# Optimization experiments

Hardware: AMD Instinct MI355X
Metric: run time of the kernel (lower is better)

## Reference

```python
import jax, jax.numpy as jnp
import numpy as np

VOCAB, HIDDEN = 128, 1024
BATCH, SEQ = 64, 512


def setup_inputs() -> dict:
    key = jax.random.key(0)
    ks = jax.random.split(key, 6)
    scale = 1.0 / np.sqrt(HIDDEN)
    return {
        "x": jax.random.randint(ks[0], (BATCH, SEQ), 0, VOCAB, dtype=jnp.int32),
        "h": jnp.zeros((BATCH, HIDDEN), dtype=jnp.float32),
        "emb": jax.random.normal(ks[1], (VOCAB, HIDDEN), dtype=jnp.float32),
        "W_hx": jax.random.normal(ks[2], (HIDDEN, HIDDEN), dtype=jnp.float32) * scale,
        "b_hx": jnp.zeros((HIDDEN,), dtype=jnp.float32),
        "W_hh": jax.random.normal(ks[3], (HIDDEN, HIDDEN), dtype=jnp.float32) * scale,
        "W_out": jax.random.normal(ks[4], (HIDDEN, VOCAB), dtype=jnp.float32) * scale,
        "b_out": jnp.zeros((VOCAB,), dtype=jnp.float32),
    }


def reference(x, h, emb, W_hx, b_hx, W_hh, W_out, b_out):
    # x: [B, S] int indices; h: [B, H] initial hidden state
    x_emb = emb[x]  # [B, S, H] embedding lookup

    def step(h, xt):  # xt: [B, H]
        h_new = jnp.tanh(xt @ W_hx + b_hx + h @ W_hh)
        return h_new, h_new

    # scan over time axis (sequential dependency on h)
    h_final, hs = jax.lax.scan(step, h, jnp.swapaxes(x_emb, 0, 1))  # hs: [S, B, H]
    out = jnp.swapaxes(hs, 0, 1)  # [B, S, H]
    logits = out @ W_out + b_out  # [B, S, V]
    return logits, h_final
```

## Files before the change

### kernel.cpp

```cpp
#include <hip/hip_runtime.h>
#include <stdint.h>
#include <stddef.h>

#define VOCAB  128
#define HIDDEN 1024
#define BATCH  64
#define SEQ    512

#define NGROUP 4
#define BG     16
#define NWG    32
#define CJ     32
#define NVW    4
#define NTHR   512

#define POISON 0x7F800000u

#define E2_OFF   0
#define WOT_OFF  131072
#define BUF_OFF  196608

typedef __attribute__((ext_vector_type(8))) short short8_t;
typedef __attribute__((ext_vector_type(4))) float f32x4;

__device__ __forceinline__ uint4 cload4u(const void* p) {
    uint4 v;
    asm volatile("global_load_dwordx4 %0, %1, off sc0 sc1" : "=v"(v) : "v"(p));
    return v;
}
__device__ __forceinline__ void cstoreu(unsigned int* p, unsigned int x) {
    asm volatile("global_store_dword %0, %1, off sc0 sc1" :: "v"(p), "v"(x) : "memory");
}
#define WAITVM0() asm volatile("s_waitcnt vmcnt(0)" ::: "memory")
#define SCHED_FENCE() __builtin_amdgcn_sched_barrier(0)

__device__ __forceinline__ unsigned short bf16_rne(float f) {
    unsigned int u = __float_as_uint(f);
    u += 0x7FFF + ((u >> 16) & 1);
    return (unsigned short)(u >> 16);
}
__device__ __forceinline__ float bf16_f32(unsigned short h) {
    return __uint_as_float(((unsigned int)h) << 16);
}

__global__ void e2_kernel(const float* __restrict__ emb, const float* __restrict__ W_hx,
                          const float* __restrict__ b_hx, float* __restrict__ E2) {
    int v = blockIdx.x >> 2;
    int j = (blockIdx.x & 3) * 256 + threadIdx.x;
    const float* er = emb + (size_t)v * HIDDEN;
    float acc = 0.f;
#pragma unroll 8
    for (int k = 0; k < HIDDEN; ++k)
        acc += er[k] * W_hx[(size_t)k * HIDDEN + j];
    E2[(size_t)v * HIDDEN + j] = acc + b_hx[j];
}

__global__ void wot_kernel(const float* __restrict__ W_out, unsigned short* __restrict__ WoT) {
    int v  = blockIdx.x;
    int k4 = threadIdx.x;
    ushort4 r;
    r.x = bf16_rne(W_out[(size_t)(k4*4+0)*VOCAB + v]);
    r.y = bf16_rne(W_out[(size_t)(k4*4+1)*VOCAB + v]);
    r.z = bf16_rne(W_out[(size_t)(k4*4+2)*VOCAB + v]);
    r.w = bf16_rne(W_out[(size_t)(k4*4+3)*VOCAB + v]);
    ((ushort4*)(WoT + (size_t)v * HIDDEN))[k4] = r;
}

__global__ void poison_kernel(unsigned int* __restrict__ bufs) {
    int i = blockIdx.x * 256 + threadIdx.x;
    ((uint4*)bufs)[i] = make_uint4(POISON, POISON, POISON, POISON);
}

extern "C" __global__ void __launch_bounds__(NTHR, 2)
rnn_kernel(const int* __restrict__ x, const float* __restrict__ h0,
           const float* __restrict__ W_hh,
           const float* __restrict__ E2, const unsigned short* __restrict__ WoT,
           const float* __restrict__ b_out,
           unsigned int* __restrict__ bufs,
           float* __restrict__ logits, float* __restrict__ hf) {
    extern __shared__ char lds_raw[];
    short* sHi  = (short*)lds_raw;
    short* sLo  = sHi + 16 * 1024;
    float* sPart = (float*)(sLo + 16 * 1024);
    int*   sX   = (int*)(sPart + 8 * 512);

    const int wg = blockIdx.x;
    const int g  = wg / NWG;
    const int w  = wg % NWG;
    const int b0 = g * BG;
    const int j0 = w * CJ;
    const int tid  = threadIdx.x;
    const int lane = tid & 63;
    const int wv   = tid >> 6;

    {
        const int4* xs4 = (const int4*)(x + (size_t)b0 * SEQ);
#pragma unroll
        for (int i = 0; i < 4; ++i)
            ((int4*)sX)[tid + 512 * i] = xs4[tid + 512 * i];
    }

    short8_t whi[2][4], wlo[2][4];
    {
        const int colb = lane & 15, kgrp = lane >> 4;
#pragma unroll
        for (int ct = 0; ct < 2; ++ct) {
            int col = j0 + ct * 16 + colb;
#pragma unroll
            for (int c = 0; c < 4; ++c) {
                int kb = wv * 128 + c * 32 + kgrp * 8;
#pragma unroll
                for (int e = 0; e < 8; ++e) {
                    float wval = W_hh[(size_t)(kb + e) * HIDDEN + col];
                    unsigned short hi = bf16_rne(wval);
                    whi[ct][c][e] = (short)hi;
                    wlo[ct][c][e] = (short)bf16_rne(wval - bf16_f32(hi));
                }
            }
        }
    }

    short8_t wvo[4];
    {
        const int colv = lane & 15, kgrp = lane >> 4;
#pragma unroll
        for (int c = 0; c < 4; ++c) {
            int kb = wv * 128 + c * 32 + kgrp * 8;
#pragma unroll
            for (int e = 0; e < 8; ++e)
                wvo[c][e] = (colv < NVW)
                    ? (short)WoT[(size_t)(w * NVW + colv) * HIDDEN + kb + e] : (short)0;
        }
    }
    const float boV = (tid < 64) ? b_out[w * NVW + (tid & 3)] : 0.f;
    __syncthreads();

    const int srow = tid >> 5;
    const int sslt = tid & 31;
    const int rb = tid >> 5, jb = tid & 31;
    const int ar = lane & 15, acg = lane >> 4;

    for (int t = 0; t < SEQ; ++t) {
        float e2p = E2[(size_t)sX[rb * SEQ + t] * HIDDEN + j0 + jb];
        if (t == 0) {
#pragma unroll
            for (int i = 0; i < 4; ++i) {
                int c = i * 32 + sslt;
                const float* p = h0 + (size_t)(b0 + srow) * HIDDEN + c * 8;
                short8_t h8, l8;
#pragma unroll
                for (int e = 0; e < 8; ++e) {
                    float vv = p[e];
                    unsigned short hi = bf16_rne(vv);
                    h8[e] = (short)hi;
                    l8[e] = (short)bf16_rne(vv - bf16_f32(hi));
                }
                int cs = (c ^ (srow & 7)) << 3;
                *(short8_t*)(sHi + srow * 1024 + cs) = h8;
                *(short8_t*)(sLo + srow * 1024 + cs) = l8;
            }
        } else {
            const unsigned int* src = bufs + ((size_t)((t - 1) & 3) << 16)
                                           + ((size_t)(b0 + srow) << 10);
            uint4 d[8];
            unsigned pend = 0xF;
            int guard = 0;
            do {
#pragma unroll
                for (int i = 0; i < 4; ++i)
                    if (pend & (1u << i)) {
                        int c = i * 32 + sslt;
                        d[2*i]   = cload4u(src + c * 8);
                        d[2*i+1] = cload4u(src + c * 8 + 4);
                    }
                WAITVM0();
                SCHED_FENCE();
#pragma unroll
                for (int i = 0; i < 4; ++i)
                    if (pend & (1u << i)) {
                        bool ok = d[2*i].x   != POISON && d[2*i].y   != POISON
                               && d[2*i].z   != POISON && d[2*i].w   != POISON
                               && d[2*i+1].x != POISON && d[2*i+1].y != POISON
                               && d[2*i+1].z != POISON && d[2*i+1].w != POISON;
                        if (ok) pend &= ~(1u << i);
                    }
                if (!pend) break;
                __builtin_amdgcn_s_sleep(1);
            } while (++guard < (1 << 20));
            SCHED_FENCE();
#pragma unroll
            for (int i = 0; i < 4; ++i) {
                int c = i * 32 + sslt;
                int cs = (c ^ (srow & 7)) << 3;
                short8_t h8, l8;
                h8[0]=(short)(d[2*i].x>>16);   l8[0]=(short)(d[2*i].x&0xFFFF);
                h8[1]=(short)(d[2*i].y>>16);   l8[1]=(short)(d[2*i].y&0xFFFF);
                h8[2]=(short)(d[2*i].z>>16);   l8[2]=(short)(d[2*i].z&0xFFFF);
                h8[3]=(short)(d[2*i].w>>16);   l8[3]=(short)(d[2*i].w&0xFFFF);
                h8[4]=(short)(d[2*i+1].x>>16); l8[4]=(short)(d[2*i+1].x&0xFFFF);
                h8[5]=(short)(d[2*i+1].y>>16); l8[5]=(short)(d[2*i+1].y&0xFFFF);
                h8[6]=(short)(d[2*i+1].z>>16); l8[6]=(short)(d[2*i+1].z&0xFFFF);
                h8[7]=(short)(d[2*i+1].w>>16); l8[7]=(short)(d[2*i+1].w&0xFFFF);
                *(short8_t*)(sHi + srow * 1024 + cs) = h8;
                *(short8_t*)(sLo + srow * 1024 + cs) = l8;
            }
        }
        __syncthreads();

        f32x4 acc0 = {0.f, 0.f, 0.f, 0.f};
        f32x4 acc1 = {0.f, 0.f, 0.f, 0.f};
#pragma unroll
        for (int c = 0; c < 4; ++c) {
            int c8 = wv * 16 + c * 4 + acg;
            int off = ar * 1024 + ((c8 ^ (ar & 7)) << 3);
            short8_t ahi = *(const short8_t*)(sHi + off);
            short8_t alo = *(const short8_t*)(sLo + off);
            acc0 = __builtin_amdgcn_mfma_f32_16x16x32_bf16(ahi, whi[0][c], acc0, 0, 0, 0);
            acc1 = __builtin_amdgcn_mfma_f32_16x16x32_bf16(ahi, whi[1][c], acc1, 0, 0, 0);
            acc0 = __builtin_amdgcn_mfma_f32_16x16x32_bf16(alo, whi[0][c], acc0, 0, 0, 0);
            acc1 = __builtin_amdgcn_mfma_f32_16x16x32_bf16(alo, whi[1][c], acc1, 0, 0, 0);
            acc0 = __builtin_amdgcn_mfma_f32_16x16x32_bf16(ahi, wlo[0][c], acc0, 0, 0, 0);
            acc1 = __builtin_amdgcn_mfma_f32_16x16x32_bf16(ahi, wlo[1][c], acc1, 0, 0, 0);
        }
#pragma unroll
        for (int q = 0; q < 4; ++q) {
            sPart[wv * 512 + (acg * 4 + q) * 32 + ar]      = acc0[q];
            sPart[wv * 512 + (acg * 4 + q) * 32 + 16 + ar] = acc1[q];
        }
        __syncthreads();

        {
            float s = 0.f;
#pragma unroll
            for (int z = 0; z < 8; ++z) s += sPart[z * 512 + tid];
            float hn = tanhf(s + e2p);
            unsigned short hi = bf16_rne(hn);
            unsigned short lo = bf16_rne(hn - bf16_f32(hi));
            unsigned int pk = ((unsigned int)hi << 16) | (unsigned int)lo;
            size_t idx = ((size_t)(b0 + rb) << 10) + j0 + jb;
            cstoreu(bufs + ((size_t)(t & 3) << 16) + idx, pk);
            cstoreu(bufs + ((size_t)((t + 2) & 3) << 16) + idx, POISON);
            if (t == SEQ - 1)
                hf[(size_t)(b0 + rb) * HIDDEN + j0 + jb] = hn;
        }
        __syncthreads();

        if (t > 0) {
            f32x4 accL = {0.f, 0.f, 0.f, 0.f};
#pragma unroll
            for (int c = 0; c < 4; ++c) {
                int c8 = wv * 16 + c * 4 + acg;
                int off = ar * 1024 + ((c8 ^ (ar & 7)) << 3);
                short8_t ahi = *(const short8_t*)(sHi + off);
                accL = __builtin_amdgcn_mfma_f32_16x16x32_bf16(ahi, wvo[c], accL, 0, 0, 0);
            }
            if (ar < NVW) {
#pragma unroll
                for (int q = 0; q < 4; ++q)
                    sPart[wv * 64 + (acg * 4 + q) * 4 + ar] = accL[q];
            }
            __syncthreads();
            if (tid < 64) {
                int b = tid >> 2, v = tid & 3;
                float s = 0.f;
#pragma unroll
                for (int z = 0; z < 8; ++z) s += sPart[z * 64 + b * 4 + v];
                logits[((size_t)(b0 + b) * SEQ + (t - 1)) * VOCAB + w * NVW + v] = s + boV;
            }
        }
    }

    {
        const unsigned int* src = bufs + ((size_t)((SEQ - 1) & 3) << 16)
                                       + ((size_t)(b0 + srow) << 10);
        uint4 d[8];
        unsigned pend = 0xF;
        int guard = 0;
        do {
#pragma unroll
            for (int i = 0; i < 4; ++i)
                if (pend & (1u << i)) {
                    int c = i * 32 + sslt;
                    d[2*i]   = cload4u(src + c * 8);
                    d[2*i+1] = cload4u(src + c * 8 + 4);
                }
            WAITVM0();
            SCHED_FENCE();
#pragma unroll
            for (int i = 0; i < 4; ++i)
                if (pend & (1u << i)) {
                    bool ok = d[2*i].x   != POISON && d[2*i].y   != POISON
                           && d[2*i].z   != POISON && d[2*i].w   != POISON
                           && d[2*i+1].x != POISON && d[2*i+1].y != POISON
                           && d[2*i+1].z != POISON && d[2*i+1].w != POISON;
                    if (ok) pend &= ~(1u << i);
                }
            if (!pend) break;
            __builtin_amdgcn_s_sleep(1);
        } while (++guard < (1 << 20));
        SCHED_FENCE();
        __syncthreads();
#pragma unroll
        for (int i = 0; i < 4; ++i) {
            int c = i * 32 + sslt;
            int cs = (c ^ (srow & 7)) << 3;
            short8_t h8;
            h8[0]=(short)(d[2*i].x>>16);   h8[1]=(short)(d[2*i].y>>16);
            h8[2]=(short)(d[2*i].z>>16);   h8[3]=(short)(d[2*i].w>>16);
            h8[4]=(short)(d[2*i+1].x>>16); h8[5]=(short)(d[2*i+1].y>>16);
            h8[6]=(short)(d[2*i+1].z>>16); h8[7]=(short)(d[2*i+1].w>>16);
            *(short8_t*)(sHi + srow * 1024 + cs) = h8;
        }
    }
    __syncthreads();
    {
        f32x4 accL = {0.f, 0.f, 0.f, 0.f};
#pragma unroll
        for (int c = 0; c < 4; ++c) {
            int c8 = wv * 16 + c * 4 + acg;
            int off = ar * 1024 + ((c8 ^ (ar & 7)) << 3);
            short8_t ahi = *(const short8_t*)(sHi + off);
            accL = __builtin_amdgcn_mfma_f32_16x16x32_bf16(ahi, wvo[c], accL, 0, 0, 0);
        }
        if (ar < NVW) {
#pragma unroll
            for (int q = 0; q < 4; ++q)
                sPart[wv * 64 + (acg * 4 + q) * 4 + ar] = accL[q];
        }
        __syncthreads();
        if (tid < 64) {
            int b = tid >> 2, v = tid & 3;
            float s = 0.f;
#pragma unroll
            for (int z = 0; z < 8; ++z) s += sPart[z * 64 + b * 4 + v];
            logits[((size_t)(b0 + b) * SEQ + (SEQ - 1)) * VOCAB + w * NVW + v] = s + boV;
        }
    }
}

extern "C" void kernel_launch(void* const* d_in, const int* in_sizes, int n_in,
                              void* d_out, int out_size, void* d_ws, size_t ws_size,
                              hipStream_t stream) {
    (void)in_sizes; (void)n_in; (void)out_size; (void)ws_size;
    const int*   x     = (const int*)  d_in[0];
    const float* h0    = (const float*)d_in[1];
    const float* emb   = (const float*)d_in[2];
    const float* W_hx  = (const float*)d_in[3];
    const float* b_hx  = (const float*)d_in[4];
    const float* W_hh  = (const float*)d_in[5];
    const float* W_out = (const float*)d_in[6];
    const float* b_out = (const float*)d_in[7];

    float* logits = (float*)d_out;
    float* hf     = logits + (size_t)BATCH * SEQ * VOCAB;

    float* ws  = (float*)d_ws;
    float* E2  = ws + E2_OFF;
    unsigned short* WoT = (unsigned short*)(ws + WOT_OFF);
    unsigned int*   bufs = (unsigned int*)(ws + BUF_OFF);

    poison_kernel<<<256, 256, 0, stream>>>(bufs);
    e2_kernel<<<512, 256, 0, stream>>>(emb, W_hx, b_hx, E2);
    wot_kernel<<<128, 256, 0, stream>>>(W_out, WoT);

    hipFuncSetAttribute(reinterpret_cast<const void*>(rnn_kernel),
                        hipFuncAttributeMaxDynamicSharedMemorySize, 114688);
    rnn_kernel<<<NGROUP * NWG, NTHR, 114688, stream>>>(x, h0, W_hh, E2, WoT, b_out,
                                                       bufs, logits, hf);
}
```

Measured before the change: 1.653 ms.

## Double-buffer hidden state in LDS and rotate logits projection across waves

Adds a second LDS buffer for the bf16 hidden-state high parts, alternating by timestep, so the previous step's state stays readable while the next one is written. This lets the per-step output projection run without its own barriers. Instead of every wave computing a partial logits sum and reducing through LDS with two extra __syncthreads, one wave (rotating by timestep) computes the full K=1024 projection from W_out held in LDS and writes logits directly. LDS use rises to about 152 KB, and one wave carries extra MFMA work each step, which may unbalance the waves.

```diff
diff --git a/kernel.cpp b/kernel.cpp
--- a/kernel.cpp
+++ b/kernel.cpp
@@ -79,10 +79,12 @@
            unsigned int* __restrict__ bufs,
            float* __restrict__ logits, float* __restrict__ hf) {
     extern __shared__ char lds_raw[];
-    short* sHi  = (short*)lds_raw;
-    short* sLo  = sHi + 16 * 1024;
-    float* sPart = (float*)(sLo + 16 * 1024);
-    int*   sX   = (int*)(sPart + 8 * 512);
+    short* sHi0 = (short*)lds_raw;
+    short* sHi1 = (short*)(lds_raw + 32768);
+    short* sLo  = (short*)(lds_raw + 65536);
+    float* sPart = (float*)(lds_raw + 98304);
+    short* sWo  = (short*)(lds_raw + 114688);
+    int*   sX   = (int*)(lds_raw + 122880);
 
     const int wg = blockIdx.x;
     const int g  = wg / NWG;
@@ -99,6 +101,11 @@
         for (int i = 0; i < 4; ++i)
             ((int4*)sX)[tid + 512 * i] = xs4[tid + 512 * i];
     }
+    {
+        int r = tid >> 7, cidx = tid & 127;
+        *(short8_t*)(sWo + r * 1024 + cidx * 8) =
+            *(const short8_t*)(WoT + (size_t)(w * NVW + r) * HIDDEN + cidx * 8);
+    }
 
     short8_t whi[2][4], wlo[2][4];
     {
@@ -120,28 +127,17 @@
         }
     }
 
-    short8_t wvo[4];
-    {
-        const int colv = lane & 15, kgrp = lane >> 4;
-#pragma unroll
-        for (int c = 0; c < 4; ++c) {
-            int kb = wv * 128 + c * 32 + kgrp * 8;
-#pragma unroll
-            for (int e = 0; e < 8; ++e)
-                wvo[c][e] = (colv < NVW)
-                    ? (short)WoT[(size_t)(w * NVW + colv) * HIDDEN + kb + e] : (short)0;
-        }
-    }
-    const float boV = (tid < 64) ? b_out[w * NVW + (tid & 3)] : 0.f;
-    __syncthreads();
-
     const int srow = tid >> 5;
     const int sslt = tid & 31;
     const int rb = tid >> 5, jb = tid & 31;
     const int ar = lane & 15, acg = lane >> 4;
+    const float boL = (ar < NVW) ? b_out[w * NVW + ar] : 0.f;
+    __syncthreads();
 
     for (int t = 0; t < SEQ; ++t) {
+        short* sHi_p = (t & 1) ? sHi1 : sHi0;
         float e2p = E2[(size_t)sX[rb * SEQ + t] * HIDDEN + j0 + jb];
+
         if (t == 0) {
 #pragma unroll
             for (int i = 0; i < 4; ++i) {
@@ -156,7 +152,7 @@
                     l8[e] = (short)bf16_rne(vv - bf16_f32(hi));
                 }
                 int cs = (c ^ (srow & 7)) << 3;
-                *(short8_t*)(sHi + srow * 1024 + cs) = h8;
+                *(short8_t*)(sHi_p + srow * 1024 + cs) = h8;
                 *(short8_t*)(sLo + srow * 1024 + cs) = l8;
             }
         } else {
@@ -201,7 +197,7 @@
                 h8[5]=(short)(d[2*i+1].y>>16); l8[5]=(short)(d[2*i+1].y&0xFFFF);
                 h8[6]=(short)(d[2*i+1].z>>16); l8[6]=(short)(d[2*i+1].z&0xFFFF);
                 h8[7]=(short)(d[2*i+1].w>>16); l8[7]=(short)(d[2*i+1].w&0xFFFF);
-                *(short8_t*)(sHi + srow * 1024 + cs) = h8;
+                *(short8_t*)(sHi_p + srow * 1024 + cs) = h8;
                 *(short8_t*)(sLo + srow * 1024 + cs) = l8;
             }
         }
@@ -213,7 +209,7 @@
         for (int c = 0; c < 4; ++c) {
             int c8 = wv * 16 + c * 4 + acg;
             int off = ar * 1024 + ((c8 ^ (ar & 7)) << 3);
-            short8_t ahi = *(const short8_t*)(sHi + off);
+            short8_t ahi = *(const short8_t*)(sHi_p + off);
             short8_t alo = *(const short8_t*)(sLo + off);
             acc0 = __builtin_amdgcn_mfma_f32_16x16x32_bf16(ahi, whi[0][c], acc0, 0, 0, 0);
             acc1 = __builtin_amdgcn_mfma_f32_16x16x32_bf16(ahi, whi[1][c], acc1, 0, 0, 0);
@@ -243,29 +239,32 @@
             if (t == SEQ - 1)
                 hf[(size_t)(b0 + rb) * HIDDEN + j0 + jb] = hn;
         }
-        __syncthreads();
-
-        if (t > 0) {
-            f32x4 accL = {0.f, 0.f, 0.f, 0.f};
-#pragma unroll
-            for (int c = 0; c < 4; ++c) {
-                int c8 = wv * 16 + c * 4 + acg;
-                int off = ar * 1024 + ((c8 ^ (ar & 7)) << 3);
-                short8_t ahi = *(const short8_t*)(sHi + off);
-                accL = __builtin_amdgcn_mfma_f32_16x16x32_bf16(ahi, wvo[c], accL, 0, 0, 0);
+
+        if (t > 0 && wv == ((t - 1) & 7)) {
+            f32x4 L0 = {0.f,0.f,0.f,0.f}, L1 = {0.f,0.f,0.f,0.f};
+            f32x4 L2 = {0.f,0.f,0.f,0.f}, L3 = {0.f,0.f,0.f,0.f};
+            const short8_t zz = {0,0,0,0,0,0,0,0};
+#pragma unroll
+            for (int kq = 0; kq < 8; ++kq) {
+#pragma unroll
+                for (int u = 0; u < 4; ++u) {
+                    int kc = kq * 4 + u;
+                    int c8 = kc * 4 + acg;
+                    short8_t a8 = *(const short8_t*)(sHi_p + ar * 1024 + ((c8 ^ (ar & 7)) << 3));
+                    short8_t b8 = (ar < NVW)
+                        ? *(const short8_t*)(sWo + ar * 1024 + kc * 32 + acg * 8) : zz;
+                    if (u == 0)      L0 = __builtin_amdgcn_mfma_f32_16x16x32_bf16(a8, b8, L0, 0, 0, 0);
+                    else if (u == 1) L1 = __builtin_amdgcn_mfma_f32_16x16x32_bf16(a8, b8, L1, 0, 0, 0);
+                    else if (u == 2) L2 = __builtin_amdgcn_mfma_f32_16x16x32_bf16(a8, b8, L2, 0, 0, 0);
+                    else             L3 = __builtin_amdgcn_mfma_f32_16x16x32_bf16(a8, b8, L3, 0, 0, 0);
+                }
             }
             if (ar < NVW) {
 #pragma unroll
-                for (int q = 0; q < 4; ++q)
-                    sPart[wv * 64 + (acg * 4 + q) * 4 + ar] = accL[q];
-            }
-            __syncthreads();
-            if (tid < 64) {
-                int b = tid >> 2, v = tid & 3;
-                float s = 0.f;
-#pragma unroll
-                for (int z = 0; z < 8; ++z) s += sPart[z * 64 + b * 4 + v];
-                logits[((size_t)(b0 + b) * SEQ + (t - 1)) * VOCAB + w * NVW + v] = s + boV;
+                for (int q = 0; q < 4; ++q) {
+                    float val = L0[q] + L1[q] + L2[q] + L3[q] + boL;
+                    logits[((size_t)(b0 + acg * 4 + q) * SEQ + (t - 1)) * VOCAB + w * NVW + ar] = val;
+                }
             }
         }
     }
@@ -299,7 +298,6 @@
             __builtin_amdgcn_s_sleep(1);
         } while (++guard < (1 << 20));
         SCHED_FENCE();
-        __syncthreads();
 #pragma unroll
         for (int i = 0; i < 4; ++i) {
             int c = i * 32 + sslt;
@@ -309,31 +307,35 @@
             h8[2]=(short)(d[2*i].z>>16);   h8[3]=(short)(d[2*i].w>>16);
             h8[4]=(short)(d[2*i+1].x>>16); h8[5]=(short)(d[2*i+1].y>>16);
             h8[6]=(short)(d[2*i+1].z>>16); h8[7]=(short)(d[2*i+1].w>>16);
-            *(short8_t*)(sHi + srow * 1024 + cs) = h8;
+            *(short8_t*)(sHi0 + srow * 1024 + cs) = h8;
         }
     }
     __syncthreads();
-    {
-        f32x4 accL = {0.f, 0.f, 0.f, 0.f};
-#pragma unroll
-        for (int c = 0; c < 4; ++c) {
-            int c8 = wv * 16 + c * 4 + acg;
-            int off = ar * 1024 + ((c8 ^ (ar & 7)) << 3);
-            short8_t ahi = *(const short8_t*)(sHi + off);
-            accL = __builtin_amdgcn_mfma_f32_16x16x32_bf16(ahi, wvo[c], accL, 0, 0, 0);
+    if (wv == ((SEQ - 1) & 7)) {
+        f32x4 L0 = {0.f,0.f,0.f,0.f}, L1 = {0.f,0.f,0.f,0.f};
+        f32x4 L2 = {0.f,0.f,0.f,0.f}, L3 = {0.f,0.f,0.f,0.f};
+        const short8_t zz = {0,0,0,0,0,0,0,0};
+#pragma unroll
+        for (int kq = 0; kq < 8; ++kq) {
+#pragma unroll
+            for (int u = 0; u < 4; ++u) {
+                int kc = kq * 4 + u;
+                int c8 = kc * 4 + acg;
+                short8_t a8 = *(const short8_t*)(sHi0 + ar * 1024 + ((c8 ^ (ar & 7)) << 3));
+                short8_t b8 = (ar < NVW)
+                    ? *(const short8_t*)(sWo + ar * 1024 + kc * 32 + acg * 8) : zz;
+                if (u == 0)      L0 = __builtin_amdgcn_mfma_f32_16x16x32_bf16(a8, b8, L0, 0, 0, 0);
+                else if (u == 1) L1 = __builtin_amdgcn_mfma_f32_16x16x32_bf16(a8, b8, L1, 0, 0, 0);
+                else if (u == 2) L2 = __builtin_amdgcn_mfma_f32_16x16x32_bf16(a8, b8, L2, 0, 0, 0);
+                else             L3 = __builtin_amdgcn_mfma_f32_16x16x32_bf16(a8, b8, L3, 0, 0, 0);
+            }
         }
         if (ar < NVW) {
 #pragma unroll
-            for (int q = 0; q < 4; ++q)
-                sPart[wv * 64 + (acg * 4 + q) * 4 + ar] = accL[q];
-        }
-        __syncthreads();
-        if (tid < 64) {
-            int b = tid >> 2, v = tid & 3;
-            float s = 0.f;
-#pragma unroll
-            for (int z = 0; z < 8; ++z) s += sPart[z * 64 + b * 4 + v];
-            logits[((size_t)(b0 + b) * SEQ + (SEQ - 1)) * VOCAB + w * NVW + v] = s + boV;
+            for (int q = 0; q < 4; ++q) {
+                float val = L0[q] + L1[q] + L2[q] + L3[q] + boL;
+                logits[((size_t)(b0 + acg * 4 + q) * SEQ + (SEQ - 1)) * VOCAB + w * NVW + ar] = val;
+            }
         }
     }
 }
@@ -364,7 +366,7 @@
     wot_kernel<<<128, 256, 0, stream>>>(W_out, WoT);
 
     hipFuncSetAttribute(reinterpret_cast<const void*>(rnn_kernel),
-                        hipFuncAttributeMaxDynamicSharedMemorySize, 114688);
-    rnn_kernel<<<NGROUP * NWG, NTHR, 114688, stream>>>(x, h0, W_hh, E2, WoT, b_out,
+                        hipFuncAttributeMaxDynamicSharedMemorySize, 155648);
+    rnn_kernel<<<NGROUP * NWG, NTHR, 155648, stream>>>(x, h0, W_hh, E2, WoT, b_out,
                                                        bufs, logits, hf);
 }
```

Result: slower. 1.814 ms (median of 2 runs) (+9.7%).

## Load hidden state directly in MFMA operand layout, bypassing LDS staging

Applied to the files above, without the earlier changes.

Each lane now polls and loads exactly the hidden-state fragments it feeds into the MFMA, so the A operands (hi and lo bf16 parts) stay in registers instead of being written to LDS, synchronized, and read back. The lo-part LDS buffer and the barrier before the recurrent matmul are removed, and the dynamic LDS allocation shrinks. The hi part is still written to LDS for the output-logits projection. Global loads for polling now use a different per-lane access pattern, which may change coalescing.

```diff
diff --git a/kernel.cpp b/kernel.cpp
--- a/kernel.cpp
+++ b/kernel.cpp
@@ -41,6 +41,21 @@
 }
 __device__ __forceinline__ float bf16_f32(unsigned short h) {
     return __uint_as_float(((unsigned int)h) << 16);
+}
+__device__ __forceinline__ bool ok8(const uint4 a, const uint4 b) {
+    return a.x != POISON && a.y != POISON && a.z != POISON && a.w != POISON
+        && b.x != POISON && b.y != POISON && b.z != POISON && b.w != POISON;
+}
+__device__ __forceinline__ void unpack8(const uint4 a, const uint4 b,
+                                        short8_t* h8, short8_t* l8) {
+    (*h8)[0]=(short)(a.x>>16); (*l8)[0]=(short)(a.x&0xFFFF);
+    (*h8)[1]=(short)(a.y>>16); (*l8)[1]=(short)(a.y&0xFFFF);
+    (*h8)[2]=(short)(a.z>>16); (*l8)[2]=(short)(a.z&0xFFFF);
+    (*h8)[3]=(short)(a.w>>16); (*l8)[3]=(short)(a.w&0xFFFF);
+    (*h8)[4]=(short)(b.x>>16); (*l8)[4]=(short)(b.x&0xFFFF);
+    (*h8)[5]=(short)(b.y>>16); (*l8)[5]=(short)(b.y&0xFFFF);
+    (*h8)[6]=(short)(b.z>>16); (*l8)[6]=(short)(b.z&0xFFFF);
+    (*h8)[7]=(short)(b.w>>16); (*l8)[7]=(short)(b.w&0xFFFF);
 }
 
 __global__ void e2_kernel(const float* __restrict__ emb, const float* __restrict__ W_hx,
@@ -80,9 +95,8 @@
            float* __restrict__ logits, float* __restrict__ hf) {
     extern __shared__ char lds_raw[];
     short* sHi  = (short*)lds_raw;
-    short* sLo  = sHi + 16 * 1024;
-    float* sPart = (float*)(sLo + 16 * 1024);
-    int*   sX   = (int*)(sPart + 8 * 512);
+    float* sPart = (float*)(lds_raw + 32768);
+    int*   sX   = (int*)(lds_raw + 49152);
 
     const int wg = blockIdx.x;
     const int g  = wg / NWG;
@@ -92,6 +106,8 @@
     const int tid  = threadIdx.x;
     const int lane = tid & 63;
     const int wv   = tid >> 6;
+    const int r    = lane & 15;
+    const int kg   = lane >> 4;
 
     {
         const int4* xs4 = (const int4*)(x + (size_t)b0 * SEQ);
@@ -102,13 +118,12 @@
 
     short8_t whi[2][4], wlo[2][4];
     {
-        const int colb = lane & 15, kgrp = lane >> 4;
 #pragma unroll
         for (int ct = 0; ct < 2; ++ct) {
-            int col = j0 + ct * 16 + colb;
+            int col = j0 + ct * 16 + r;
 #pragma unroll
             for (int c = 0; c < 4; ++c) {
-                int kb = wv * 128 + c * 32 + kgrp * 8;
+                int kb = wv * 128 + c * 32 + kg * 8;
 #pragma unroll
                 for (int e = 0; e < 8; ++e) {
                     float wval = W_hh[(size_t)(kb + e) * HIDDEN + col];
@@ -122,110 +137,85 @@
 
     short8_t wvo[4];
     {
-        const int colv = lane & 15, kgrp = lane >> 4;
 #pragma unroll
         for (int c = 0; c < 4; ++c) {
-            int kb = wv * 128 + c * 32 + kgrp * 8;
+            int kb = wv * 128 + c * 32 + kg * 8;
 #pragma unroll
             for (int e = 0; e < 8; ++e)
-                wvo[c][e] = (colv < NVW)
-                    ? (short)WoT[(size_t)(w * NVW + colv) * HIDDEN + kb + e] : (short)0;
+                wvo[c][e] = (r < NVW)
+                    ? (short)WoT[(size_t)(w * NVW + r) * HIDDEN + kb + e] : (short)0;
         }
     }
     const float boV = (tid < 64) ? b_out[w * NVW + (tid & 3)] : 0.f;
+    const int rb = tid >> 5, jb = tid & 31;
     __syncthreads();
-
-    const int srow = tid >> 5;
-    const int sslt = tid & 31;
-    const int rb = tid >> 5, jb = tid & 31;
-    const int ar = lane & 15, acg = lane >> 4;
 
     for (int t = 0; t < SEQ; ++t) {
         float e2p = E2[(size_t)sX[rb * SEQ + t] * HIDDEN + j0 + jb];
+
+        short8_t ahi[4], alo[4];
         if (t == 0) {
-#pragma unroll
-            for (int i = 0; i < 4; ++i) {
-                int c = i * 32 + sslt;
-                const float* p = h0 + (size_t)(b0 + srow) * HIDDEN + c * 8;
-                short8_t h8, l8;
+            const float* hr = h0 + ((size_t)(b0 + r) << 10) + wv * 128 + kg * 8;
+#pragma unroll
+            for (int c = 0; c < 4; ++c) {
+                float4 f0 = *(const float4*)(hr + c * 32);
+                float4 f1 = *(const float4*)(hr + c * 32 + 4);
+                float fv[8] = {f0.x,f0.y,f0.z,f0.w,f1.x,f1.y,f1.z,f1.w};
 #pragma unroll
                 for (int e = 0; e < 8; ++e) {
-                    float vv = p[e];
-                    unsigned short hi = bf16_rne(vv);
-                    h8[e] = (short)hi;
-                    l8[e] = (short)bf16_rne(vv - bf16_f32(hi));
+                    unsigned short hi = bf16_rne(fv[e]);
+                    ahi[c][e] = (short)hi;
+                    alo[c][e] = (short)bf16_rne(fv[e] - bf16_f32(hi));
                 }
-                int cs = (c ^ (srow & 7)) << 3;
-                *(short8_t*)(sHi + srow * 1024 + cs) = h8;
-                *(short8_t*)(sLo + srow * 1024 + cs) = l8;
             }
         } else {
             const unsigned int* src = bufs + ((size_t)((t - 1) & 3) << 16)
-                                           + ((size_t)(b0 + srow) << 10);
-            uint4 d[8];
+                                           + ((size_t)(b0 + r) << 10) + wv * 128 + kg * 8;
+            uint4 d0a,d0b,d1a,d1b,d2a,d2b,d3a,d3b;
             unsigned pend = 0xF;
             int guard = 0;
             do {
-#pragma unroll
-                for (int i = 0; i < 4; ++i)
-                    if (pend & (1u << i)) {
-                        int c = i * 32 + sslt;
-                        d[2*i]   = cload4u(src + c * 8);
-                        d[2*i+1] = cload4u(src + c * 8 + 4);
-                    }
+                if (pend & 1u) { d0a = cload4u(src +  0); d0b = cload4u(src +  4); }
+                if (pend & 2u) { d1a = cload4u(src + 32); d1b = cload4u(src + 36); }
+                if (pend & 4u) { d2a = cload4u(src + 64); d2b = cload4u(src + 68); }
+                if (pend & 8u) { d3a = cload4u(src + 96); d3b = cload4u(src + 100); }
                 WAITVM0();
                 SCHED_FENCE();
-#pragma unroll
-                for (int i = 0; i < 4; ++i)
-                    if (pend & (1u << i)) {
-                        bool ok = d[2*i].x   != POISON && d[2*i].y   != POISON
-                               && d[2*i].z   != POISON && d[2*i].w   != POISON
-                               && d[2*i+1].x != POISON && d[2*i+1].y != POISON
-                               && d[2*i+1].z != POISON && d[2*i+1].w != POISON;
-                        if (ok) pend &= ~(1u << i);
-                    }
+                if ((pend & 1u) && ok8(d0a, d0b)) pend &= ~1u;
+                if ((pend & 2u) && ok8(d1a, d1b)) pend &= ~2u;
+                if ((pend & 4u) && ok8(d2a, d2b)) pend &= ~4u;
+                if ((pend & 8u) && ok8(d3a, d3b)) pend &= ~8u;
                 if (!pend) break;
                 __builtin_amdgcn_s_sleep(1);
             } while (++guard < (1 << 20));
             SCHED_FENCE();
-#pragma unroll
-            for (int i = 0; i < 4; ++i) {
-                int c = i * 32 + sslt;
-                int cs = (c ^ (srow & 7)) << 3;
-                short8_t h8, l8;
-                h8[0]=(short)(d[2*i].x>>16);   l8[0]=(short)(d[2*i].x&0xFFFF);
-                h8[1]=(short)(d[2*i].y>>16);   l8[1]=(short)(d[2*i].y&0xFFFF);
-                h8[2]=(short)(d[2*i].z>>16);   l8[2]=(short)(d[2*i].z&0xFFFF);
-                h8[3]=(short)(d[2*i].w>>16);   l8[3]=(short)(d[2*i].w&0xFFFF);
-                h8[4]=(short)(d[2*i+1].x>>16); l8[4]=(short)(d[2*i+1].x&0xFFFF);
-                h8[5]=(short)(d[2*i+1].y>>16); l8[5]=(short)(d[2*i+1].y&0xFFFF);
-                h8[6]=(short)(d[2*i+1].z>>16); l8[6]=(short)(d[2*i+1].z&0xFFFF);
-                h8[7]=(short)(d[2*i+1].w>>16); l8[7]=(short)(d[2*i+1].w&0xFFFF);
-                *(short8_t*)(sHi + srow * 1024 + cs) = h8;
-                *(short8_t*)(sLo + srow * 1024 + cs) = l8;
-            }
-        }
-        __syncthreads();
+            unpack8(d0a, d0b, &ahi[0], &alo[0]);
+            unpack8(d1a, d1b, &ahi[1], &alo[1]);
+            unpack8(d2a, d2b, &ahi[2], &alo[2]);
+            unpack8(d3a, d3b, &ahi[3], &alo[3]);
+        }
+
+#pragma unroll
+        for (int c = 0; c < 4; ++c) {
+            int c8 = wv * 16 + c * 4 + kg;
+            *(short8_t*)(sHi + r * 1024 + ((c8 ^ (r & 7)) << 3)) = ahi[c];
+        }
 
         f32x4 acc0 = {0.f, 0.f, 0.f, 0.f};
         f32x4 acc1 = {0.f, 0.f, 0.f, 0.f};
 #pragma unroll
         for (int c = 0; c < 4; ++c) {
-            int c8 = wv * 16 + c * 4 + acg;
-            int off = ar * 1024 + ((c8 ^ (ar & 7)) << 3);
-            short8_t ahi = *(const short8_t*)(sHi + off);
-            short8_t alo = *(const short8_t*)(sLo + off);
-            acc0 = __builtin_amdgcn_mfma_f32_16x16x32_bf16(ahi, whi[0][c], acc0, 0, 0, 0);
-            acc1 = __builtin_amdgcn_mfma_f32_16x16x32_bf16(ahi, whi[1][c], acc1, 0, 0, 0);
-            acc0 = __builtin_amdgcn_mfma_f32_16x16x32_bf16(alo, whi[0][c], acc0, 0, 0, 0);
-            acc1 = __builtin_amdgcn_mfma_f32_16x16x32_bf16(alo, whi[1][c], acc1, 0, 0, 0);
-            acc0 = __builtin_amdgcn_mfma_f32_16x16x32_bf16(ahi, wlo[0][c], acc0, 0, 0, 0);
-            acc1 = __builtin_amdgcn_mfma_f32_16x16x32_bf16(ahi, wlo[1][c], acc1, 0, 0, 0);
+            acc0 = __builtin_amdgcn_mfma_f32_16x16x32_bf16(ahi[c], whi[0][c], acc0, 0, 0, 0);
+            acc1 = __builtin_amdgcn_mfma_f32_16x16x32_bf16(ahi[c], whi[1][c], acc1, 0, 0, 0);
+            acc0 = __builtin_amdgcn_mfma_f32_16x16x32_bf16(alo[c], whi[0][c], acc0, 0, 0, 0);
+            acc1 = __builtin_amdgcn_mfma_f32_16x16x32_bf16(alo[c], whi[1][c], acc1, 0, 0, 0);
+            acc0 = __builtin_amdgcn_mfma_f32_16x16x32_bf16(ahi[c], wlo[0][c], acc0, 0, 0, 0);
+            acc1 = __builtin_amdgcn_mfma_f32_16x16x32_bf16(ahi[c], wlo[1][c], acc1, 0, 0, 0);
         }
 #pragma unroll
         for (int q = 0; q < 4; ++q) {
-            sPart[wv * 512 + (acg * 4 + q) * 32 + ar]      = acc0[q];
-            sPart[wv * 512 + (acg * 4 + q) * 32 + 16 + ar] = acc1[q];
+            sPart[wv * 512 + (kg * 4 + q) * 32 + r]      = acc0[q];
+            sPart[wv * 512 + (kg * 4 + q) * 32 + 16 + r] = acc1[q];
         }
         __syncthreads();
 
@@ -249,15 +239,14 @@
             f32x4 accL = {0.f, 0.f, 0.f, 0.f};
 #pragma unroll
             for (int c = 0; c < 4; ++c) {
-                int c8 = wv * 16 + c * 4 + acg;
-                int off = ar * 1024 + ((c8 ^ (ar & 7)) << 3);
-                short8_t ahi = *(const short8_t*)(sHi + off);
-                accL = __builtin_amdgcn_mfma_f32_16x16x32_bf16(ahi, wvo[c], accL, 0, 0, 0);
-            }
-            if (ar < NVW) {
+                int c8 = wv * 16 + c * 4 + kg;
+                short8_t a8 = *(const short8_t*)(sHi + r * 1024 + ((c8 ^ (r & 7)) << 3));
+                accL = __builtin_amdgcn_mfma_f32_16x16x32_bf16(a8, wvo[c], accL, 0, 0, 0);
+            }
+            if (r < NVW) {
 #pragma unroll
                 for (int q = 0; q < 4; ++q)
-                    sPart[wv * 64 + (acg * 4 + q) * 4 + ar] = accL[q];
+                    sPart[wv * 64 + (kg * 4 + q) * 4 + r] = accL[q];
             }
             __syncthreads();
             if (tid < 64) {
@@ -272,60 +261,48 @@
 
     {
         const unsigned int* src = bufs + ((size_t)((SEQ - 1) & 3) << 16)
-                                       + ((size_t)(b0 + srow) << 10);
-        uint4 d[8];
+                                       + ((size_t)(b0 + r) << 10) + wv * 128 + kg * 8;
+        uint4 d0a,d0b,d1a,d1b,d2a,d2b,d3a,d3b;
         unsigned pend = 0xF;
         int guard = 0;
         do {
-#pragma unroll
-            for (int i = 0; i < 4; ++i)
-                if (pend & (1u << i)) {
-                    int c = i * 32 + sslt;
-                    d[2*i]   = cload4u(src + c * 8);
-                    d[2*i+1] = cload4u(src + c * 8 + 4);
-                }
+            if (pend & 1u) { d0a = cload4u(src +  0); d0b = cload4u(src +  4); }
+            if (pend & 2u) { d1a = cload4u(src + 32); d1b = cload4u(src + 36); }
+            if (pend & 4u) { d2a = cload4u(src + 64); d2b = cload4u(src + 68); }
+            if (pend & 8u) { d3a = cload4u(src + 96); d3b = cload4u(src + 100); }
             WAITVM0();
             SCHED_FENCE();
-#pragma unroll
-            for (int i = 0; i < 4; ++i)
-                if (pend & (1u << i)) {
-                    bool ok = d[2*i].x   != POISON && d[2*i].y   != POISON
-                           && d[2*i].z   != POISON && d[2*i].w   != POISON
-                           && d[2*i+1].x != POISON && d[2*i+1].y != POISON
-                           && d[2*i+1].z != POISON && d[2*i+1].w != POISON;
-                    if (ok) pend &= ~(1u << i);
-                }
+            if ((pend & 1u) && ok8(d0a, d0b)) pend &= ~1u;
+            if ((pend & 2u) && ok8(d1a, d1b)) pend &= ~2u;
+            if ((pend & 4u) && ok8(d2a, d2b)) pend &= ~4u;
+            if ((pend & 8u) && ok8(d3a, d3b)) pend &= ~8u;
             if (!pend) break;
             __builtin_amdgcn_s_sleep(1);
         } while (++guard < (1 << 20));
         SCHED_FENCE();
-        __syncthreads();
-#pragma unroll
-        for (int i = 0; i < 4; ++i) {
-            int c = i * 32 + sslt;
-            int cs = (c ^ (srow & 7)) << 3;
-            short8_t h8;
-            h8[0]=(short)(d[2*i].x>>16);   h8[1]=(short)(d[2*i].y>>16);
-            h8[2]=(short)(d[2*i].z>>16);   h8[3]=(short)(d[2*i].w>>16);
-            h8[4]=(short)(d[2*i+1].x>>16); h8[5]=(short)(d[2*i+1].y>>16);
-            h8[6]=(short)(d[2*i+1].z>>16); h8[7]=(short)(d[2*i+1].w>>16);
-            *(short8_t*)(sHi + srow * 1024 + cs) = h8;
-        }
+        short8_t h8, l8;
+        unpack8(d0a, d0b, &h8, &l8);
+        *(short8_t*)(sHi + r * 1024 + (((wv * 16 + 0 * 4 + kg) ^ (r & 7)) << 3)) = h8;
+        unpack8(d1a, d1b, &h8, &l8);
+        *(short8_t*)(sHi + r * 1024 + (((wv * 16 + 1 * 4 + kg) ^ (r & 7)) << 3)) = h8;
+        unpack8(d2a, d2b, &h8, &l8);
+        *(short8_t*)(sHi + r * 1024 + (((wv * 16 + 2 * 4 + kg) ^ (r & 7)) << 3)) = h8;
+        unpack8(d3a, d3b, &h8, &l8);
+        *(short8_t*)(sHi + r * 1024 + (((wv * 16 + 3 * 4 + kg) ^ (r & 7)) << 3)) = h8;
     }
     __syncthreads();
     {
         f32x4 accL = {0.f, 0.f, 0.f, 0.f};
 #pragma unroll
         for (int c = 0; c < 4; ++c) {
-            int c8 = wv * 16 + c * 4 + acg;
-            int off = ar * 1024 + ((c8 ^ (ar & 7)) << 3);
-            short8_t ahi = *(const short8_t*)(sHi + off);
-            accL = __builtin_amdgcn_mfma_f32_16x16x32_bf16(ahi, wvo[c], accL, 0, 0, 0);
-        }
-        if (ar < NVW) {
+            int c8 = wv * 16 + c * 4 + kg;
+            short8_t a8 = *(const short8_t*)(sHi + r * 1024 + ((c8 ^ (r & 7)) << 3));
+            accL = __builtin_amdgcn_mfma_f32_16x16x32_bf16(a8, wvo[c], accL, 0, 0, 0);
+        }
+        if (r < NVW) {
 #pragma unroll
             for (int q = 0; q < 4; ++q)
-                sPart[wv * 64 + (acg * 4 + q) * 4 + ar] = accL[q];
+                sPart[wv * 64 + (kg * 4 + q) * 4 + r] = accL[q];
         }
         __syncthreads();
         if (tid < 64) {
@@ -364,7 +341,7 @@
     wot_kernel<<<128, 256, 0, stream>>>(W_out, WoT);
 
     hipFuncSetAttribute(reinterpret_cast<const void*>(rnn_kernel),
-                        hipFuncAttributeMaxDynamicSharedMemorySize, 114688);
-    rnn_kernel<<<NGROUP * NWG, NTHR, 114688, stream>>>(x, h0, W_hh, E2, WoT, b_out,
-                                                       bufs, logits, hf);
-}
+                        hipFuncAttributeMaxDynamicSharedMemorySize, 81920);
+    rnn_kernel<<<NGROUP * NWG, NTHR, 81920, stream>>>(x, h0, W_hh, E2, WoT, b_out,
+                                                      bufs, logits, hf);
+}
```

After: 1.849 ms. +11.9%, slower.
